# Kernel optimization log

Hardware: AMD Instinct MI355X
Metric: run time of the kernel (lower is better)

The kernel has to match this reference:

```python
import jax, jax.numpy as jnp
import numpy as np

DT = 0.1  # integration step
EPS = 1e-06

def setup_inputs() -> dict:
    key = jax.random.key(0)
    ks = jax.random.split(key, 8)
    B, T, I, H, O = 256, 512, 64, 512, 64
    return {
        'x_seq': jax.random.normal(ks[0], (B, T, I), jnp.float32),
        'W_in0': jax.random.normal(ks[1], (H, I), jnp.float32) * (1.0 / np.sqrt(I)),
        'b_in0': jnp.zeros((H,), jnp.float32),
        'A0':    jax.random.normal(ks[2], (H, H), jnp.float32) * 0.1,
        'tau0':  jnp.ones((H,), jnp.float32),
        'W_in1': jax.random.normal(ks[3], (H, H), jnp.float32) * (1.0 / np.sqrt(H)),
        'b_in1': jnp.zeros((H,), jnp.float32),
        'A1':    jax.random.normal(ks[4], (H, H), jnp.float32) * 0.1,
        'tau1':  jnp.ones((H,), jnp.float32),
        'W_out': jax.random.normal(ks[5], (O, H), jnp.float32) * (1.0 / np.sqrt(H)),
        'b_out': jnp.zeros((O,), jnp.float32),
    }

def _euler(h, drive, A, tau):
    # dh/dt = (1/|tau|+eps) * (-h + tanh(h @ A.T + drive)); Euler step
    inv_tau = 1.0 / (jnp.abs(tau) + EPS)
    dh = inv_tau * (-h + jnp.tanh(h @ A.T + drive))
    return h + DT * dh

def reference(x_seq, W_in0, b_in0, A0, tau0, W_in1, b_in1, A1, tau1, W_out, b_out):
    B, T, _ = x_seq.shape
    H = A0.shape[0]
    # layer-0 input projection is time-independent of hidden state: precompute
    xw = jnp.einsum('bti,hi->bth', x_seq, W_in0) + b_in0  # (B, T, H)

    def step(carry, xw_t):
        h0, h1 = carry
        h0 = _euler(h0, xw_t, A0, tau0)
        h1 = _euler(h1, h0 @ W_in1.T + b_in1, A1, tau1)
        y = h1 @ W_out.T + b_out
        return (h0, h1), y

    h0 = jnp.zeros((B, H), x_seq.dtype)
    h1 = jnp.zeros((B, H), x_seq.dtype)
    _, ys = jax.lax.scan(step, (h0, h1), jnp.swapaxes(xw, 0, 1))  # scan over time
    return jnp.swapaxes(ys, 0, 1)  # (B, T, O)
```

## Files before the change

kernel.cpp:

```cpp
#include <hip/hip_runtime.h>
#include <hip/hip_bf16.h>
#include <stdint.h>

#define B_ 256
#define T_ 512
#define I_ 64
#define H_ 512
#define O_ 64
#define DT_ 0.1f
#define EPS_ 1e-6f
#define SCALE_ 2048.0f
#define INVSCALE_ 4.8828125e-4f

typedef _Float16 f16x8 __attribute__((ext_vector_type(8)));
typedef float    f32x4 __attribute__((ext_vector_type(4)));

__device__ __forceinline__ f32x4 mfma16(f16x8 a, f16x8 b, f32x4 c) {
    return __builtin_amdgcn_mfma_f32_16x16x32_f16(a, b, c, 0, 0, 0);
}
__device__ __forceinline__ float fast_tanh(float x) {
    float e = __expf(2.0f * x);
    return 1.0f - 2.0f / (e + 1.0f);
}
__device__ __forceinline__ bool is_f32_input(const void* tau0) {
    return *(const unsigned int*)tau0 == 0x3F800000u;
}
__device__ __forceinline__ float load_any(const void* p, int i, bool f32) {
    return f32 ? ((const float*)p)[i] : (float)((const __bf16*)p)[i];
}
__device__ __forceinline__ _Float16 f16bits(unsigned short u) {
    union { unsigned short u; _Float16 f; } c; c.u = u; return c.f;
}
__device__ __forceinline__ unsigned short bits16(_Float16 f) {
    union { unsigned short u; _Float16 f; } c; c.f = f; return c.u;
}
__device__ __forceinline__ int bsum8(uint32_t v) {
    return (int)((v & 0xFF) + ((v >> 8) & 0xFF) + ((v >> 16) & 0xFF) + ((v >> 24) & 0xFF));
}
__device__ __forceinline__ int bmax8(uint32_t v) {
    int a = (int)(v & 0xFF), b = (int)((v >> 8) & 0xFF);
    int c = (int)((v >> 16) & 0xFF), d = (int)((v >> 24) & 0xFF);
    int x = a > b ? a : b, y = c > d ? c : d;
    return x > y ? x : y;
}

#define WS_A0H 0u
#define WS_A1H 524288u
#define WS_W1H 1048576u
#define WS_A0L 1572864u
#define WS_A1L 2097152u
#define WS_W1L 2621440u
#define WS_W0H 3145728u
#define WS_W0L 3211264u
#define WS_WOP 3276800u
#define WS_IT0 3407872u
#define WS_IT1 3409920u
#define WS_BI0 3411968u
#define WS_BI1 3414016u
#define WS_BO  3416064u
#define WS_FLGP 3538944u
#define WS_XCD2 3604480u
#define WS_HB0  4194304u
#define WS_HB1  5242880u

__global__ void k_swizzle(const void* __restrict__ src, _Float16* __restrict__ hi,
                          _Float16* __restrict__ lo, int NK, int kshift,
                          const void* __restrict__ tau) {
    bool f32 = is_f32_input(tau);
    int i = blockIdx.x * 256 + threadIdx.x;
    if (i >= NK) return;
    int n = i >> kshift;
    int k = i & ((1 << kshift) - 1);
    float v = load_any(src, i, f32);
    _Float16 h = (_Float16)v;
    _Float16 l = (_Float16)((v - (float)h) * SCALE_);
    int tile = n >> 4, m = n & 15, kk = k >> 5, q = (k >> 3) & 3, j = k & 7;
    int Kst = 1 << (kshift - 5);
    int off = ((tile * Kst + kk) << 9) + (((q << 4) | m) << 3) + j;
    hi[off] = h;
    lo[off] = l;
}

__global__ void k_swzwo(const void* __restrict__ src, _Float16* __restrict__ dst,
                        const void* __restrict__ tau) {
    bool f32 = is_f32_input(tau);
    int i = blockIdx.x * 256 + threadIdx.x;
    if (i >= 65536) return;
    int j = i & 7, l = (i >> 3) & 63, kk = (i >> 9) & 15, cg = i >> 13;
    int m = l & 15, q = l >> 4;
    int k = kk * 32 + q * 8 + j;
    float v = (m < 8) ? load_any(src, (8 * cg + m) * H_ + k, f32) : 0.0f;
    dst[i] = (_Float16)v;
}

__global__ void k_params(const void* t0, const void* t1,
                         const void* b0, const void* b1, const void* bo,
                         float* it0, float* it1, float* b0f, float* b1f, float* bof) {
    bool f32 = is_f32_input(t0);
    int i = threadIdx.x;
    if (i < H_) {
        it0[i] = 1.0f / (fabsf(load_any(t0, i, f32)) + EPS_);
        it1[i] = 1.0f / (fabsf(load_any(t1, i, f32)) + EPS_);
        b0f[i] = load_any(b0, i, f32);
        b1f[i] = load_any(b1, i, f32);
    }
    if (i < O_) bof[i] = load_any(bo, i, f32);
}

__global__ void k_zero(uint32_t* p, int n) {
    int i = blockIdx.x * 256 + threadIdx.x;
    if (i < n) p[i] = 0;
}

__device__ __forceinline__ void waitflag(const uint32_t* p, uint32_t tgt) {
    while (__hip_atomic_load(p, __ATOMIC_RELAXED, __HIP_MEMORY_SCOPE_AGENT) < tgt)
        __builtin_amdgcn_s_sleep(1);
    __asm__ __volatile__("" ::: "memory");
}

__global__ __launch_bounds__(256, 1) void liquid_kernel(
    const void* __restrict__ x_seq, const void* __restrict__ tau0probe,
    char* __restrict__ ws, void* __restrict__ out)
{
    __shared__ _Float16 hAh[16][520], hAl[16][520];
    __shared__ _Float16 hBh[16][520], hBl[16][520];
    __shared__ float yscr[4][16][16];
    __shared__ int s_fast;

    const bool f32 = is_f32_input(tau0probe);
    const int tid  = threadIdx.x;
    const int lane = tid & 63;
    const int w    = tid >> 6;
    const int m    = lane & 15;
    const int q    = lane >> 4;
    const int koff = q * 8;
    const int rg   = blockIdx.x;
    const int cg   = blockIdx.y;
    const int chain = blockIdx.z;
    const int r0   = rg * 16;
    const int colg = cg * 64 + w * 16 + m;
    const int tlg  = cg * 4 + w;
    const int c0   = w * 128 + lane;
    const int c1   = c0 + 64;

    uint32_t* ring = (uint32_t*)(ws + WS_HB0);
    uint32_t* hb1  = (uint32_t*)(ws + WS_HB1);
    uint32_t* fpad = (uint32_t*)(ws + WS_FLGP);
    uint32_t* fsf  = fpad +         (size_t)rg * 8 * 32;
    uint32_t* f1f  = fpad + 4096  + (size_t)rg * 8 * 32;
    uint32_t* pg0  = fpad + 8192  + (size_t)rg * 8 * 32;
    uint32_t* pg1  = fpad + 12288 + (size_t)rg * 8 * 32;

    {
        uint32_t* xc = (uint32_t*)(ws + WS_XCD2) + (size_t)rg * 32;
        if (tid == 0) {
            int xid = (int)(__builtin_amdgcn_s_getreg((3u << 11) | 20u) & 7u);
            __hip_atomic_fetch_add(xc + (xid >> 2), 1u << (8 * (xid & 3)),
                                   __ATOMIC_RELAXED, __HIP_MEMORY_SCOPE_AGENT);
            uint32_t v0, v1;
            do {
                __builtin_amdgcn_s_sleep(1);
                v0 = __hip_atomic_load(xc,     __ATOMIC_RELAXED, __HIP_MEMORY_SCOPE_AGENT);
                v1 = __hip_atomic_load(xc + 1, __ATOMIC_RELAXED, __HIP_MEMORY_SCOPE_AGENT);
            } while (bsum8(v0) + bsum8(v1) < 16);
            int mx0 = bmax8(v0), mx1 = bmax8(v1);
            s_fast = ((mx0 > mx1 ? mx0 : mx1) == 16) ? 1 : 0;
        }
    }

    const float* bow = (const float*)(ws + WS_BO);
    const float boY  = (m < 8) ? bow[cg * 8 + m] : 0.0f;

    __syncthreads();
    const bool fastp = (s_fast != 0);

    if (chain == 0) {
        const float it0c = ((const float*)(ws + WS_IT0))[colg];
        const float bi0c = ((const float*)(ws + WS_BI0))[colg];
        const size_t fb  = (((size_t)(tlg * 16)) << 9) + (lane << 3);
        const size_t fb0 = (((size_t)(tlg * 2))  << 9) + (lane << 3);
        f16x8 cA0h[16], cA0l[16];
#pragma unroll
        for (int kk = 0; kk < 16; ++kk) {
            cA0h[kk] = *(const f16x8*)((const _Float16*)(ws + WS_A0H) + fb + ((size_t)kk << 9));
            cA0l[kk] = *(const f16x8*)((const _Float16*)(ws + WS_A0L) + fb + ((size_t)kk << 9));
        }
        f16x8 cW0h[2], cW0l[2];
#pragma unroll
        for (int kk = 0; kk < 2; ++kk) {
            cW0h[kk] = *(const f16x8*)((const _Float16*)(ws + WS_W0H) + fb0 + ((size_t)kk << 9));
            cW0l[kk] = *(const f16x8*)((const _Float16*)(ws + WS_W0L) + fb0 + ((size_t)kk << 9));
        }
        const float*  xpf = (const float*) x_seq + (size_t)(r0 + m) * T_ * I_ + koff;
        const __bf16* xpb = (const __bf16*)x_seq + (size_t)(r0 + m) * T_ * I_ + koff;
        float h0m[4] = {0.f, 0.f, 0.f, 0.f};

        f32x4 xf0 = {}, xf1 = {}, xf2 = {}, xf3 = {};
        uint4 xb0 = {}, xb1 = {};
        if (f32) {
            xf0 = *(const f32x4*)(xpf);
            xf1 = *(const f32x4*)(xpf + 4);
            xf2 = *(const f32x4*)(xpf + 32);
            xf3 = *(const f32x4*)(xpf + 36);
        } else {
            xb0 = *(const uint4*)(xpb);
            xb1 = *(const uint4*)(xpb + 32);
        }

        for (int s = 0; s < T_; ++s) {
            waitflag(fsf + (size_t)(2 * w) * 32,     4u * (uint32_t)s);
            waitflag(fsf + (size_t)(2 * w + 1) * 32, 4u * (uint32_t)s);
            uint32_t rv0[16], rv1[16];
            {
                const uint32_t* src = ring + ((size_t)((s & 1) * 16 + rg) * 16) * 512;
                if (fastp) {
#pragma unroll
                    for (int k = 0; k < 16; ++k) {
                        rv0[k] = src[(size_t)k * 512 + c0];
                        rv1[k] = src[(size_t)k * 512 + c1];
                    }
                } else {
#pragma unroll
                    for (int k = 0; k < 16; ++k) {
                        rv0[k] = __hip_atomic_load(src + (size_t)k * 512 + c0, __ATOMIC_RELAXED, __HIP_MEMORY_SCOPE_AGENT);
                        rv1[k] = __hip_atomic_load(src + (size_t)k * 512 + c1, __ATOMIC_RELAXED, __HIP_MEMORY_SCOPE_AGENT);
                    }
                }
            }
            __syncthreads();
#pragma unroll
            for (int k = 0; k < 16; ++k) {
                hAh[k][c0] = f16bits((unsigned short)(rv0[k] & 0xFFFFu));
                hAl[k][c0] = f16bits((unsigned short)(rv0[k] >> 16));
                hAh[k][c1] = f16bits((unsigned short)(rv1[k] & 0xFFFFu));
                hAl[k][c1] = f16bits((unsigned short)(rv1[k] >> 16));
            }
            if (lane == 0)
                __hip_atomic_fetch_add(pg0 + (size_t)cg * 32, 1u, __ATOMIC_RELAXED, __HIP_MEMORY_SCOPE_AGENT);
            __syncthreads();

            f32x4 a1 = {0.f,0.f,0.f,0.f}, a2 = {0.f,0.f,0.f,0.f}, a3 = {0.f,0.f,0.f,0.f};
#pragma unroll
            for (int kk = 0; kk < 16; ++kk) {
                f16x8 ah = *(const f16x8*)(&hAh[m][kk * 32 + koff]);
                f16x8 al = *(const f16x8*)(&hAl[m][kk * 32 + koff]);
                a1 = mfma16(ah, cA0h[kk], a1);
                a2 = mfma16(ah, cA0l[kk], a2);
                a3 = mfma16(al, cA0h[kk], a3);
            }
            {
                f16x8 xh0, xl0, xh1, xl1;
                if (f32) {
                    float v0[8] = {xf0[0],xf0[1],xf0[2],xf0[3],xf1[0],xf1[1],xf1[2],xf1[3]};
                    float v1[8] = {xf2[0],xf2[1],xf2[2],xf2[3],xf3[0],xf3[1],xf3[2],xf3[3]};
#pragma unroll
                    for (int j = 0; j < 8; ++j) {
                        xh0[j] = (_Float16)v0[j];
                        xl0[j] = (_Float16)((v0[j] - (float)xh0[j]) * SCALE_);
                        xh1[j] = (_Float16)v1[j];
                        xl1[j] = (_Float16)((v1[j] - (float)xh1[j]) * SCALE_);
                    }
                } else {
                    const __bf16* p0 = (const __bf16*)&xb0;
                    const __bf16* p1 = (const __bf16*)&xb1;
#pragma unroll
                    for (int j = 0; j < 8; ++j) {
                        xh0[j] = (_Float16)(float)p0[j]; xl0[j] = (_Float16)0.0f;
                        xh1[j] = (_Float16)(float)p1[j]; xl1[j] = (_Float16)0.0f;
                    }
                }
                a1 = mfma16(xh0, cW0h[0], a1);
                a2 = mfma16(xh0, cW0l[0], a2);
                a3 = mfma16(xl0, cW0h[0], a3);
                a1 = mfma16(xh1, cW0h[1], a1);
                a2 = mfma16(xh1, cW0l[1], a2);
                a3 = mfma16(xl1, cW0h[1], a3);
            }

            if (s > 0) {
                uint32_t tgt = (lane < 8) ? 4u * (uint32_t)s : 4u * (uint32_t)(s - 1);
                const uint32_t* pp = (lane < 8) ? (pg0 + (size_t)lane * 32)
                                                : (pg1 + (size_t)(lane - 8) * 32);
                uint32_t v = (lane < 16)
                    ? __hip_atomic_load(pp, __ATOMIC_RELAXED, __HIP_MEMORY_SCOPE_AGENT)
                    : 0xFFFFFFFFu;
                while (__any(v < tgt)) {
                    __builtin_amdgcn_s_sleep(1);
                    v = (lane < 16)
                        ? __hip_atomic_load(pp, __ATOMIC_RELAXED, __HIP_MEMORY_SCOPE_AGENT)
                        : 0xFFFFFFFFu;
                }
                __asm__ __volatile__("" ::: "memory");
            }

            uint32_t* dst = ring + ((size_t)(((s + 1) & 1) * 16 + rg) * 16) * 512 + colg;
#pragma unroll
            for (int r = 0; r < 4; ++r) {
                float z = a1[r] + (a2[r] + a3[r]) * INVSCALE_ + bi0c;
                float h = h0m[r];
                h += DT_ * it0c * (fast_tanh(z) - h);
                h0m[r] = h;
                _Float16 hh = (_Float16)h;
                _Float16 hl = (_Float16)((h - (float)hh) * SCALE_);
                uint32_t pk = (uint32_t)bits16(hh) | ((uint32_t)bits16(hl) << 16);
                if (fastp) dst[(size_t)(q * 4 + r) * 512] = pk;
                else __hip_atomic_store(dst + (size_t)(q * 4 + r) * 512, pk,
                                        __ATOMIC_RELAXED, __HIP_MEMORY_SCOPE_AGENT);
            }
            asm volatile("s_waitcnt vmcnt(0)" ::: "memory");
            if (lane == 0)
                __hip_atomic_fetch_add(fsf + (size_t)cg * 32, 1u, __ATOMIC_RELAXED, __HIP_MEMORY_SCOPE_AGENT);

            {
                const int tn = (s + 1 < T_) ? s + 1 : s;
                if (f32) {
                    const float* p = xpf + (size_t)tn * I_;
                    xf0 = *(const f32x4*)(p);
                    xf1 = *(const f32x4*)(p + 4);
                    xf2 = *(const f32x4*)(p + 32);
                    xf3 = *(const f32x4*)(p + 36);
                } else {
                    const __bf16* p = xpb + (size_t)tn * I_;
                    xb0 = *(const uint4*)(p);
                    xb1 = *(const uint4*)(p + 32);
                }
            }
        }
        return;
    }

    {
        const float it1c = ((const float*)(ws + WS_IT1))[colg];
        const float bi1c = ((const float*)(ws + WS_BI1))[colg];
        const size_t fb = (((size_t)(tlg * 16)) << 9) + (lane << 3);
        f16x8 cA1h[16], cA1l[16], cW1h[16], cW1l[16];
#pragma unroll
        for (int kk = 0; kk < 16; ++kk) {
            cA1h[kk] = *(const f16x8*)((const _Float16*)(ws + WS_A1H) + fb + ((size_t)kk << 9));
            cA1l[kk] = *(const f16x8*)((const _Float16*)(ws + WS_A1L) + fb + ((size_t)kk << 9));
            cW1h[kk] = *(const f16x8*)((const _Float16*)(ws + WS_W1H) + fb + ((size_t)kk << 9));
            cW1l[kk] = *(const f16x8*)((const _Float16*)(ws + WS_W1L) + fb + ((size_t)kk << 9));
        }
        const _Float16* pWOP = (const _Float16*)(ws + WS_WOP) + (((size_t)(cg * 16)) << 9) + (lane << 3);
        float h1m[4] = {0.f, 0.f, 0.f, 0.f};

        for (int s = 0; s < T_; ++s) {
            waitflag(f1f + (size_t)(2 * w) * 32,     4u * (uint32_t)s);
            waitflag(f1f + (size_t)(2 * w + 1) * 32, 4u * (uint32_t)s);
            uint32_t rv0[16], rv1[16];
            {
                const uint32_t* src = hb1 + ((size_t)((s & 1) * 16 + rg) * 16) * 512;
                if (fastp) {
#pragma unroll
                    for (int k = 0; k < 16; ++k) {
                        rv0[k] = src[(size_t)k * 512 + c0];
                        rv1[k] = src[(size_t)k * 512 + c1];
                    }
                } else {
#pragma unroll
                    for (int k = 0; k < 16; ++k) {
                        rv0[k] = __hip_atomic_load(src + (size_t)k * 512 + c0, __ATOMIC_RELAXED, __HIP_MEMORY_SCOPE_AGENT);
                        rv1[k] = __hip_atomic_load(src + (size_t)k * 512 + c1, __ATOMIC_RELAXED, __HIP_MEMORY_SCOPE_AGENT);
                    }
                }
            }
            waitflag(fsf + (size_t)(2 * w) * 32,     4u * (uint32_t)(s + 1));
            waitflag(fsf + (size_t)(2 * w + 1) * 32, 4u * (uint32_t)(s + 1));
#pragma unroll
            for (int k = 0; k < 16; ++k) {
                hAh[k][c0] = f16bits((unsigned short)(rv0[k] & 0xFFFFu));
                hAl[k][c0] = f16bits((unsigned short)(rv0[k] >> 16));
                hAh[k][c1] = f16bits((unsigned short)(rv1[k] & 0xFFFFu));
                hAl[k][c1] = f16bits((unsigned short)(rv1[k] >> 16));
            }
            __syncthreads();

            {
                const uint32_t* src = ring + ((size_t)(((s + 1) & 1) * 16 + rg) * 16) * 512;
                if (fastp) {
#pragma unroll
                    for (int k = 0; k < 16; ++k) {
                        rv0[k] = src[(size_t)k * 512 + c0];
                        rv1[k] = src[(size_t)k * 512 + c1];
                    }
                } else {
#pragma unroll
                    for (int k = 0; k < 16; ++k) {
                        rv0[k] = __hip_atomic_load(src + (size_t)k * 512 + c0, __ATOMIC_RELAXED, __HIP_MEMORY_SCOPE_AGENT);
                        rv1[k] = __hip_atomic_load(src + (size_t)k * 512 + c1, __ATOMIC_RELAXED, __HIP_MEMORY_SCOPE_AGENT);
                    }
                }
            }

            if (s >= 1) {
                f32x4 y1 = {0.f,0.f,0.f,0.f}, y2 = {0.f,0.f,0.f,0.f};
#pragma unroll
                for (int kk2 = 0; kk2 < 4; ++kk2) {
                    int kk = w * 4 + kk2;
                    f16x8 ah = *(const f16x8*)(&hAh[m][kk * 32 + koff]);
                    f16x8 al = *(const f16x8*)(&hAl[m][kk * 32 + koff]);
                    f16x8 b  = *(const f16x8*)(pWOP + ((size_t)kk << 9));
                    y1 = mfma16(ah, b, y1);
                    y2 = mfma16(al, b, y2);
                }
#pragma unroll
                for (int r = 0; r < 4; ++r)
                    yscr[w][q * 4 + r][m] = y1[r] + y2[r] * INVSCALE_;
            }

            f32x4 a1 = {0.f,0.f,0.f,0.f}, a2 = {0.f,0.f,0.f,0.f}, a3 = {0.f,0.f,0.f,0.f};
#pragma unroll
            for (int kk = 0; kk < 16; ++kk) {
                f16x8 ah = *(const f16x8*)(&hAh[m][kk * 32 + koff]);
                f16x8 al = *(const f16x8*)(&hAl[m][kk * 32 + koff]);
                a1 = mfma16(ah, cA1h[kk], a1);
                a2 = mfma16(ah, cA1l[kk], a2);
                a3 = mfma16(al, cA1h[kk], a3);
            }

#pragma unroll
            for (int k = 0; k < 16; ++k) {
                hBh[k][c0] = f16bits((unsigned short)(rv0[k] & 0xFFFFu));
                hBl[k][c0] = f16bits((unsigned short)(rv0[k] >> 16));
                hBh[k][c1] = f16bits((unsigned short)(rv1[k] & 0xFFFFu));
                hBl[k][c1] = f16bits((unsigned short)(rv1[k] >> 16));
            }
            if (lane == 0)
                __hip_atomic_fetch_add(pg1 + (size_t)cg * 32, 1u, __ATOMIC_RELAXED, __HIP_MEMORY_SCOPE_AGENT);
            __syncthreads();

            if (w == 0 && s >= 1 && m < 8) {
#pragma unroll
                for (int r = 0; r < 4; ++r) {
                    float v = yscr[0][q * 4 + r][m] + yscr[1][q * 4 + r][m]
                            + yscr[2][q * 4 + r][m] + yscr[3][q * 4 + r][m] + boY;
                    size_t idx = ((size_t)(r0 + q * 4 + r) * T_ + (s - 1)) * O_ + cg * 8 + m;
                    if (f32) ((float*)out)[idx] = v;
                    else     ((__bf16*)out)[idx] = (__bf16)v;
                }
            }

#pragma unroll
            for (int kk = 0; kk < 16; ++kk) {
                f16x8 ah = *(const f16x8*)(&hBh[m][kk * 32 + koff]);
                f16x8 al = *(const f16x8*)(&hBl[m][kk * 32 + koff]);
                a1 = mfma16(ah, cW1h[kk], a1);
                a2 = mfma16(ah, cW1l[kk], a2);
                a3 = mfma16(al, cW1h[kk], a3);
            }

            uint32_t* dst = hb1 + ((size_t)(((s + 1) & 1) * 16 + rg) * 16) * 512 + colg;
#pragma unroll
            for (int r = 0; r < 4; ++r) {
                float z = a1[r] + (a2[r] + a3[r]) * INVSCALE_ + bi1c;
                float h = h1m[r];
                h += DT_ * it1c * (fast_tanh(z) - h);
                h1m[r] = h;
                _Float16 hh = (_Float16)h;
                _Float16 hl = (_Float16)((h - (float)hh) * SCALE_);
                uint32_t pk = (uint32_t)bits16(hh) | ((uint32_t)bits16(hl) << 16);
                if (fastp) dst[(size_t)(q * 4 + r) * 512] = pk;
                else __hip_atomic_store(dst + (size_t)(q * 4 + r) * 512, pk,
                                        __ATOMIC_RELAXED, __HIP_MEMORY_SCOPE_AGENT);
            }
            asm volatile("s_waitcnt vmcnt(0)" ::: "memory");
            if (lane == 0)
                __hip_atomic_fetch_add(f1f + (size_t)cg * 32, 1u, __ATOMIC_RELAXED, __HIP_MEMORY_SCOPE_AGENT);
        }

        waitflag(f1f + (size_t)(2 * w) * 32,     4u * (uint32_t)T_);
        waitflag(f1f + (size_t)(2 * w + 1) * 32, 4u * (uint32_t)T_);
        {
            uint32_t rv0[16], rv1[16];
            const uint32_t* src = hb1 + ((size_t)((T_ & 1) * 16 + rg) * 16) * 512;
            if (fastp) {
#pragma unroll
                for (int k = 0; k < 16; ++k) {
                    rv0[k] = src[(size_t)k * 512 + c0];
                    rv1[k] = src[(size_t)k * 512 + c1];
                }
            } else {
#pragma unroll
                for (int k = 0; k < 16; ++k) {
                    rv0[k] = __hip_atomic_load(src + (size_t)k * 512 + c0, __ATOMIC_RELAXED, __HIP_MEMORY_SCOPE_AGENT);
                    rv1[k] = __hip_atomic_load(src + (size_t)k * 512 + c1, __ATOMIC_RELAXED, __HIP_MEMORY_SCOPE_AGENT);
                }
            }
            __syncthreads();
#pragma unroll
            for (int k = 0; k < 16; ++k) {
                hAh[k][c0] = f16bits((unsigned short)(rv0[k] & 0xFFFFu));
                hAl[k][c0] = f16bits((unsigned short)(rv0[k] >> 16));
                hAh[k][c1] = f16bits((unsigned short)(rv1[k] & 0xFFFFu));
                hAl[k][c1] = f16bits((unsigned short)(rv1[k] >> 16));
            }
        }
        __syncthreads();
        {
            f32x4 y1 = {0.f,0.f,0.f,0.f}, y2 = {0.f,0.f,0.f,0.f};
#pragma unroll
            for (int kk2 = 0; kk2 < 4; ++kk2) {
                int kk = w * 4 + kk2;
                f16x8 ah = *(const f16x8*)(&hAh[m][kk * 32 + koff]);
                f16x8 al = *(const f16x8*)(&hAl[m][kk * 32 + koff]);
                f16x8 b  = *(const f16x8*)(pWOP + ((size_t)kk << 9));
                y1 = mfma16(ah, b, y1);
                y2 = mfma16(al, b, y2);
            }
#pragma unroll
            for (int r = 0; r < 4; ++r)
                yscr[w][q * 4 + r][m] = y1[r] + y2[r] * INVSCALE_;
        }
        __syncthreads();
        if (w == 0 && m < 8) {
#pragma unroll
            for (int r = 0; r < 4; ++r) {
                float v = yscr[0][q * 4 + r][m] + yscr[1][q * 4 + r][m]
                        + yscr[2][q * 4 + r][m] + yscr[3][q * 4 + r][m] + boY;
                size_t idx = ((size_t)(r0 + q * 4 + r) * T_ + (T_ - 1)) * O_ + cg * 8 + m;
                if (f32) ((float*)out)[idx] = v;
                else     ((__bf16*)out)[idx] = (__bf16)v;
            }
        }
    }
}

extern "C" void kernel_launch(void* const* d_in, const int* in_sizes, int n_in,
                              void* d_out, int out_size, void* d_ws, size_t ws_size,
                              hipStream_t stream) {
    const void* x_seq = d_in[0];
    const void* W_in0 = d_in[1];
    const void* b_in0 = d_in[2];
    const void* A0    = d_in[3];
    const void* tau0  = d_in[4];
    const void* W_in1 = d_in[5];
    const void* b_in1 = d_in[6];
    const void* A1    = d_in[7];
    const void* tau1  = d_in[8];
    const void* W_out = d_in[9];
    const void* b_out = d_in[10];

    char* ws = (char*)d_ws;
    const int HH = H_ * H_, HI = H_ * I_;

    k_swizzle<<<(HH + 255) / 256, 256, 0, stream>>>(A0,    (_Float16*)(ws + WS_A0H), (_Float16*)(ws + WS_A0L), HH, 9, tau0);
    k_swizzle<<<(HH + 255) / 256, 256, 0, stream>>>(A1,    (_Float16*)(ws + WS_A1H), (_Float16*)(ws + WS_A1L), HH, 9, tau0);
    k_swizzle<<<(HH + 255) / 256, 256, 0, stream>>>(W_in1, (_Float16*)(ws + WS_W1H), (_Float16*)(ws + WS_W1L), HH, 9, tau0);
    k_swizzle<<<(HI + 255) / 256, 256, 0, stream>>>(W_in0, (_Float16*)(ws + WS_W0H), (_Float16*)(ws + WS_W0L), HI, 6, tau0);
    k_swzwo <<<65536 / 256, 256, 0, stream>>>(W_out, (_Float16*)(ws + WS_WOP), tau0);
    k_params<<<1, 512, 0, stream>>>(tau0, tau1, b_in0, b_in1, b_out,
                                    (float*)(ws + WS_IT0), (float*)(ws + WS_IT1),
                                    (float*)(ws + WS_BI0), (float*)(ws + WS_BI1),
                                    (float*)(ws + WS_BO));
    k_zero<<<(16896 + 255) / 256, 256, 0, stream>>>((uint32_t*)(ws + WS_FLGP), 16896);
    k_zero<<<(524288 + 255) / 256, 256, 0, stream>>>((uint32_t*)(ws + WS_HB0), 524288);

    liquid_kernel<<<dim3(16, 8, 2), dim3(256), 0, stream>>>(x_seq, tau0, ws, d_out);
}
```

Measured before the change: 3.220 ms.

## Deepen layer-0 ring to four slots and relax cross-chain handshakes

The layer-0 hidden-state ring grows from two to four slots, so the layer-0 chain only waits on layer-1 progress three steps back, and the pg0 progress counter with its handshake is removed. The LDS tile buffers become a double-buffered pair, which lets layer 0 write its tile before a single barrier instead of two. Spin-wait loops drop s_sleep, and the output store moves after the flag increment to shorten the critical path. The cost is more workspace to zero, busier polling that adds memory traffic, and a subtler correctness argument for buffer reuse.

```diff
diff --git a/kernel.cpp b/kernel.cpp
--- a/kernel.cpp
+++ b/kernel.cpp
@@ -61,7 +61,7 @@
 #define WS_FLGP 3538944u
 #define WS_XCD2 3604480u
 #define WS_HB0  4194304u
-#define WS_HB1  5242880u
+#define WS_HB1  6291456u
 
 __global__ void k_swizzle(const void* __restrict__ src, _Float16* __restrict__ hi,
                           _Float16* __restrict__ lo, int NK, int kshift,
@@ -113,8 +113,7 @@
 }
 
 __device__ __forceinline__ void waitflag(const uint32_t* p, uint32_t tgt) {
-    while (__hip_atomic_load(p, __ATOMIC_RELAXED, __HIP_MEMORY_SCOPE_AGENT) < tgt)
-        __builtin_amdgcn_s_sleep(1);
+    while (__hip_atomic_load(p, __ATOMIC_RELAXED, __HIP_MEMORY_SCOPE_AGENT) < tgt) { }
     __asm__ __volatile__("" ::: "memory");
 }
 
@@ -122,8 +121,7 @@
     const void* __restrict__ x_seq, const void* __restrict__ tau0probe,
     char* __restrict__ ws, void* __restrict__ out)
 {
-    __shared__ _Float16 hAh[16][520], hAl[16][520];
-    __shared__ _Float16 hBh[16][520], hBl[16][520];
+    __shared__ _Float16 hTh[2][16][520], hTl[2][16][520];
     __shared__ float yscr[4][16][16];
     __shared__ int s_fast;
 
@@ -148,7 +146,6 @@
     uint32_t* fpad = (uint32_t*)(ws + WS_FLGP);
     uint32_t* fsf  = fpad +         (size_t)rg * 8 * 32;
     uint32_t* f1f  = fpad + 4096  + (size_t)rg * 8 * 32;
-    uint32_t* pg0  = fpad + 8192  + (size_t)rg * 8 * 32;
     uint32_t* pg1  = fpad + 12288 + (size_t)rg * 8 * 32;
 
     {
@@ -208,11 +205,15 @@
         }
 
         for (int s = 0; s < T_; ++s) {
+            const int cur = s & 1;
+            const int rs4 = s & 3;
+            const int ws4 = (s + 1) & 3;
+
             waitflag(fsf + (size_t)(2 * w) * 32,     4u * (uint32_t)s);
             waitflag(fsf + (size_t)(2 * w + 1) * 32, 4u * (uint32_t)s);
             uint32_t rv0[16], rv1[16];
             {
-                const uint32_t* src = ring + ((size_t)((s & 1) * 16 + rg) * 16) * 512;
+                const uint32_t* src = ring + ((size_t)(rs4 * 16 + rg) * 16) * 512;
                 if (fastp) {
 #pragma unroll
                     for (int k = 0; k < 16; ++k) {
@@ -227,23 +228,20 @@
                     }
                 }
             }
+#pragma unroll
+            for (int k = 0; k < 16; ++k) {
+                hTh[cur][k][c0] = f16bits((unsigned short)(rv0[k] & 0xFFFFu));
+                hTl[cur][k][c0] = f16bits((unsigned short)(rv0[k] >> 16));
+                hTh[cur][k][c1] = f16bits((unsigned short)(rv1[k] & 0xFFFFu));
+                hTl[cur][k][c1] = f16bits((unsigned short)(rv1[k] >> 16));
+            }
             __syncthreads();
-#pragma unroll
-            for (int k = 0; k < 16; ++k) {
-                hAh[k][c0] = f16bits((unsigned short)(rv0[k] & 0xFFFFu));
-                hAl[k][c0] = f16bits((unsigned short)(rv0[k] >> 16));
-                hAh[k][c1] = f16bits((unsigned short)(rv1[k] & 0xFFFFu));
-                hAl[k][c1] = f16bits((unsigned short)(rv1[k] >> 16));
-            }
-            if (lane == 0)
-                __hip_atomic_fetch_add(pg0 + (size_t)cg * 32, 1u, __ATOMIC_RELAXED, __HIP_MEMORY_SCOPE_AGENT);
-            __syncthreads();
 
             f32x4 a1 = {0.f,0.f,0.f,0.f}, a2 = {0.f,0.f,0.f,0.f}, a3 = {0.f,0.f,0.f,0.f};
 #pragma unroll
             for (int kk = 0; kk < 16; ++kk) {
-                f16x8 ah = *(const f16x8*)(&hAh[m][kk * 32 + koff]);
-                f16x8 al = *(const f16x8*)(&hAl[m][kk * 32 + koff]);
+                f16x8 ah = *(const f16x8*)(&hTh[cur][m][kk * 32 + koff]);
+                f16x8 al = *(const f16x8*)(&hTl[cur][m][kk * 32 + koff]);
                 a1 = mfma16(ah, cA0h[kk], a1);
                 a2 = mfma16(ah, cA0l[kk], a2);
                 a3 = mfma16(al, cA0h[kk], a3);
@@ -277,23 +275,21 @@
                 a3 = mfma16(xl1, cW0h[1], a3);
             }
 
-            if (s > 0) {
-                uint32_t tgt = (lane < 8) ? 4u * (uint32_t)s : 4u * (uint32_t)(s - 1);
-                const uint32_t* pp = (lane < 8) ? (pg0 + (size_t)lane * 32)
-                                                : (pg1 + (size_t)(lane - 8) * 32);
-                uint32_t v = (lane < 16)
+            if (s >= 3) {
+                const uint32_t tgt = 4u * (uint32_t)(s - 3);
+                const uint32_t* pp = pg1 + (size_t)(lane & 7) * 32;
+                uint32_t v = (lane < 8)
                     ? __hip_atomic_load(pp, __ATOMIC_RELAXED, __HIP_MEMORY_SCOPE_AGENT)
                     : 0xFFFFFFFFu;
                 while (__any(v < tgt)) {
-                    __builtin_amdgcn_s_sleep(1);
-                    v = (lane < 16)
+                    v = (lane < 8)
                         ? __hip_atomic_load(pp, __ATOMIC_RELAXED, __HIP_MEMORY_SCOPE_AGENT)
                         : 0xFFFFFFFFu;
                 }
                 __asm__ __volatile__("" ::: "memory");
             }
 
-            uint32_t* dst = ring + ((size_t)(((s + 1) & 1) * 16 + rg) * 16) * 512 + colg;
+            uint32_t* dst = ring + ((size_t)(ws4 * 16 + rg) * 16) * 512 + colg;
 #pragma unroll
             for (int r = 0; r < 4; ++r) {
                 float z = a1[r] + (a2[r] + a3[r]) * INVSCALE_ + bi0c;
@@ -345,11 +341,14 @@
         float h1m[4] = {0.f, 0.f, 0.f, 0.f};
 
         for (int s = 0; s < T_; ++s) {
+            const int cur = s & 1, nxt = (s + 1) & 1;
+            const int rs4 = (s + 1) & 3;
+
             waitflag(f1f + (size_t)(2 * w) * 32,     4u * (uint32_t)s);
             waitflag(f1f + (size_t)(2 * w + 1) * 32, 4u * (uint32_t)s);
             uint32_t rv0[16], rv1[16];
             {
-                const uint32_t* src = hb1 + ((size_t)((s & 1) * 16 + rg) * 16) * 512;
+                const uint32_t* src = hb1 + ((size_t)(cur * 16 + rg) * 16) * 512;
                 if (fastp) {
 #pragma unroll
                     for (int k = 0; k < 16; ++k) {
@@ -368,15 +367,15 @@
             waitflag(fsf + (size_t)(2 * w + 1) * 32, 4u * (uint32_t)(s + 1));
 #pragma unroll
             for (int k = 0; k < 16; ++k) {
-                hAh[k][c0] = f16bits((unsigned short)(rv0[k] & 0xFFFFu));
-                hAl[k][c0] = f16bits((unsigned short)(rv0[k] >> 16));
-                hAh[k][c1] = f16bits((unsigned short)(rv1[k] & 0xFFFFu));
-                hAl[k][c1] = f16bits((unsigned short)(rv1[k] >> 16));
+                hTh[0][k][c0] = f16bits((unsigned short)(rv0[k] & 0xFFFFu));
+                hTl[0][k][c0] = f16bits((unsigned short)(rv0[k] >> 16));
+                hTh[0][k][c1] = f16bits((unsigned short)(rv1[k] & 0xFFFFu));
+                hTl[0][k][c1] = f16bits((unsigned short)(rv1[k] >> 16));
             }
             __syncthreads();
 
             {
-                const uint32_t* src = ring + ((size_t)(((s + 1) & 1) * 16 + rg) * 16) * 512;
+                const uint32_t* src = ring + ((size_t)(rs4 * 16 + rg) * 16) * 512;
                 if (fastp) {
 #pragma unroll
                     for (int k = 0; k < 16; ++k) {
@@ -397,8 +396,8 @@
 #pragma unroll
                 for (int kk2 = 0; kk2 < 4; ++kk2) {
                     int kk = w * 4 + kk2;
-                    f16x8 ah = *(const f16x8*)(&hAh[m][kk * 32 + koff]);
-                    f16x8 al = *(const f16x8*)(&hAl[m][kk * 32 + koff]);
+                    f16x8 ah = *(const f16x8*)(&hTh[0][m][kk * 32 + koff]);
+                    f16x8 al = *(const f16x8*)(&hTl[0][m][kk * 32 + koff]);
                     f16x8 b  = *(const f16x8*)(pWOP + ((size_t)kk << 9));
                     y1 = mfma16(ah, b, y1);
                     y2 = mfma16(al, b, y2);
@@ -411,8 +410,8 @@
             f32x4 a1 = {0.f,0.f,0.f,0.f}, a2 = {0.f,0.f,0.f,0.f}, a3 = {0.f,0.f,0.f,0.f};
 #pragma unroll
             for (int kk = 0; kk < 16; ++kk) {
-                f16x8 ah = *(const f16x8*)(&hAh[m][kk * 32 + koff]);
-                f16x8 al = *(const f16x8*)(&hAl[m][kk * 32 + koff]);
+                f16x8 ah = *(const f16x8*)(&hTh[0][m][kk * 32 + koff]);
+                f16x8 al = *(const f16x8*)(&hTl[0][m][kk * 32 + koff]);
                 a1 = mfma16(ah, cA1h[kk], a1);
                 a2 = mfma16(ah, cA1l[kk], a2);
                 a3 = mfma16(al, cA1h[kk], a3);
@@ -420,36 +419,25 @@
 
 #pragma unroll
             for (int k = 0; k < 16; ++k) {
-                hBh[k][c0] = f16bits((unsigned short)(rv0[k] & 0xFFFFu));
-                hBl[k][c0] = f16bits((unsigned short)(rv0[k] >> 16));
-                hBh[k][c1] = f16bits((unsigned short)(rv1[k] & 0xFFFFu));
-                hBl[k][c1] = f16bits((unsigned short)(rv1[k] >> 16));
+                hTh[1][k][c0] = f16bits((unsigned short)(rv0[k] & 0xFFFFu));
+                hTl[1][k][c0] = f16bits((unsigned short)(rv0[k] >> 16));
+                hTh[1][k][c1] = f16bits((unsigned short)(rv1[k] & 0xFFFFu));
+                hTl[1][k][c1] = f16bits((unsigned short)(rv1[k] >> 16));
             }
             if (lane == 0)
                 __hip_atomic_fetch_add(pg1 + (size_t)cg * 32, 1u, __ATOMIC_RELAXED, __HIP_MEMORY_SCOPE_AGENT);
             __syncthreads();
 
-            if (w == 0 && s >= 1 && m < 8) {
-#pragma unroll
-                for (int r = 0; r < 4; ++r) {
-                    float v = yscr[0][q * 4 + r][m] + yscr[1][q * 4 + r][m]
-                            + yscr[2][q * 4 + r][m] + yscr[3][q * 4 + r][m] + boY;
-                    size_t idx = ((size_t)(r0 + q * 4 + r) * T_ + (s - 1)) * O_ + cg * 8 + m;
-                    if (f32) ((float*)out)[idx] = v;
-                    else     ((__bf16*)out)[idx] = (__bf16)v;
-                }
-            }
-
 #pragma unroll
             for (int kk = 0; kk < 16; ++kk) {
-                f16x8 ah = *(const f16x8*)(&hBh[m][kk * 32 + koff]);
-                f16x8 al = *(const f16x8*)(&hBl[m][kk * 32 + koff]);
+                f16x8 ah = *(const f16x8*)(&hTh[1][m][kk * 32 + koff]);
+                f16x8 al = *(const f16x8*)(&hTl[1][m][kk * 32 + koff]);
                 a1 = mfma16(ah, cW1h[kk], a1);
                 a2 = mfma16(ah, cW1l[kk], a2);
                 a3 = mfma16(al, cW1h[kk], a3);
             }
 
-            uint32_t* dst = hb1 + ((size_t)(((s + 1) & 1) * 16 + rg) * 16) * 512 + colg;
+            uint32_t* dst = hb1 + ((size_t)(nxt * 16 + rg) * 16) * 512 + colg;
 #pragma unroll
             for (int r = 0; r < 4; ++r) {
                 float z = a1[r] + (a2[r] + a3[r]) * INVSCALE_ + bi1c;
@@ -466,6 +454,17 @@
             asm volatile("s_waitcnt vmcnt(0)" ::: "memory");
             if (lane == 0)
                 __hip_atomic_fetch_add(f1f + (size_t)cg * 32, 1u, __ATOMIC_RELAXED, __HIP_MEMORY_SCOPE_AGENT);
+
+            if (w == 0 && s >= 1 && m < 8) {
+#pragma unroll
+                for (int r = 0; r < 4; ++r) {
+                    float v = yscr[0][q * 4 + r][m] + yscr[1][q * 4 + r][m]
+                            + yscr[2][q * 4 + r][m] + yscr[3][q * 4 + r][m] + boY;
+                    size_t idx = ((size_t)(r0 + q * 4 + r) * T_ + (s - 1)) * O_ + cg * 8 + m;
+                    if (f32) ((float*)out)[idx] = v;
+                    else     ((__bf16*)out)[idx] = (__bf16)v;
+                }
+            }
         }
 
         waitflag(f1f + (size_t)(2 * w) * 32,     4u * (uint32_t)T_);
@@ -489,10 +488,10 @@
             __syncthreads();
 #pragma unroll
             for (int k = 0; k < 16; ++k) {
-                hAh[k][c0] = f16bits((unsigned short)(rv0[k] & 0xFFFFu));
-                hAl[k][c0] = f16bits((unsigned short)(rv0[k] >> 16));
-                hAh[k][c1] = f16bits((unsigned short)(rv1[k] & 0xFFFFu));
-                hAl[k][c1] = f16bits((unsigned short)(rv1[k] >> 16));
+                hTh[0][k][c0] = f16bits((unsigned short)(rv0[k] & 0xFFFFu));
+                hTl[0][k][c0] = f16bits((unsigned short)(rv0[k] >> 16));
+                hTh[0][k][c1] = f16bits((unsigned short)(rv1[k] & 0xFFFFu));
+                hTl[0][k][c1] = f16bits((unsigned short)(rv1[k] >> 16));
             }
         }
         __syncthreads();
@@ -501,8 +500,8 @@
 #pragma unroll
             for (int kk2 = 0; kk2 < 4; ++kk2) {
                 int kk = w * 4 + kk2;
-                f16x8 ah = *(const f16x8*)(&hAh[m][kk * 32 + koff]);
-                f16x8 al = *(const f16x8*)(&hAl[m][kk * 32 + koff]);
+                f16x8 ah = *(const f16x8*)(&hTh[0][m][kk * 32 + koff]);
+                f16x8 al = *(const f16x8*)(&hTl[0][m][kk * 32 + koff]);
                 f16x8 b  = *(const f16x8*)(pWOP + ((size_t)kk << 9));
                 y1 = mfma16(ah, b, y1);
                 y2 = mfma16(al, b, y2);
@@ -553,7 +552,7 @@
                                     (float*)(ws + WS_BI0), (float*)(ws + WS_BI1),
                                     (float*)(ws + WS_BO));
     k_zero<<<(16896 + 255) / 256, 256, 0, stream>>>((uint32_t*)(ws + WS_FLGP), 16896);
-    k_zero<<<(524288 + 255) / 256, 256, 0, stream>>>((uint32_t*)(ws + WS_HB0), 524288);
+    k_zero<<<(786432 + 255) / 256, 256, 0, stream>>>((uint32_t*)(ws + WS_HB0), 786432);
 
     liquid_kernel<<<dim3(16, 8, 2), dim3(256), 0, stream>>>(x_seq, tau0, ws, d_out);
 }
```

Result: faster. 3.056 ms (-5.1%).
